# Performance work log

Hardware: AMD Instinct MI355X
Metric: run time of the kernel (lower is better)

## Reference

```python
import jax, jax.numpy as jnp
import numpy as np

N = 10000
E = 160000
F_IN = 64
HID = 128
HEADS = 8
NC = 3
NEG_SLOPE = 0.2
EPS = 1e-16


def setup_inputs() -> dict:
    key = jax.random.key(0)
    ks = jax.random.split(key, 12)
    p = lambda k, shape: jax.random.normal(k, shape, jnp.float32) * 0.1
    return {
        "x": jax.random.normal(ks[0], (N, F_IN), jnp.float32),
        "edge_index": jax.random.randint(ks[1], (2, E), 0, N),
        # conv1: F_IN -> 8 heads x 128, concat -> 1024
        "W1": p(ks[2], (F_IN, HEADS * HID)),
        "a_src1": p(ks[3], (HEADS, HID)),
        "a_dst1": p(ks[4], (HEADS, HID)),
        "b1": jnp.zeros((HEADS * HID,), jnp.float32),
        # conv2: 1024 -> 8 heads x 64, concat -> 512
        "W2": p(ks[5], (HEADS * HID, HEADS * (HID // 2))),
        "a_src2": p(ks[6], (HEADS, HID // 2)),
        "a_dst2": p(ks[7], (HEADS, HID // 2)),
        "b2": jnp.zeros((HEADS * (HID // 2),), jnp.float32),
        # conv3: 512 -> 1 head x 3, mean (concat=False)
        "W3": p(ks[8], (HEADS * (HID // 2), NC)),
        "a_src3": p(ks[9], (1, NC)),
        "a_dst3": p(ks[10], (1, NC)),
        "b3": jnp.zeros((NC,), jnp.float32),
    }


def gat_conv(x, src, dst, W, a_src, a_dst, b, concat):
    """PyG-style GATConv (eval mode, self-loops already in src/dst)."""
    n = x.shape[0]
    H, C = a_src.shape
    h = (x @ W).reshape(n, H, C)                      # [N, H, C]
    s_src = jnp.sum(h * a_src[None], axis=-1)         # [N, H]
    s_dst = jnp.sum(h * a_dst[None], axis=-1)         # [N, H]
    e = jax.nn.leaky_relu(s_src[src] + s_dst[dst], NEG_SLOPE)  # [E, H]
    # segment softmax over incoming edges per destination node
    m = jax.ops.segment_max(e, dst, num_segments=n)   # [N, H]
    ex = jnp.exp(e - m[dst])
    denom = jax.ops.segment_sum(ex, dst, num_segments=n)
    alpha = ex / (denom[dst] + EPS)                   # [E, H]
    msg = h[src] * alpha[:, :, None]                  # [E, H, C]
    out = jax.ops.segment_sum(msg, dst, num_segments=n)  # [N, H, C]
    out = out.reshape(n, H * C) if concat else out.mean(axis=1)
    return out + b


def reference(x, edge_index, W1, a_src1, a_dst1, b1, W2, a_src2, a_dst2, b2, W3, a_src3, a_dst3, b3):
    n = x.shape[0]
    loop = jnp.arange(n, dtype=edge_index.dtype)
    src = jnp.concatenate([edge_index[0], loop])
    dst = jnp.concatenate([edge_index[1], loop])
    h = gat_conv(x, src, dst, W1, a_src1, a_dst1, b1, True)
    h = jax.nn.elu(h)
    h = gat_conv(h, src, dst, W2, a_src2, a_dst2, b2, True)
    h = jax.nn.elu(h)
    h = gat_conv(h, src, dst, W3, a_src3, a_dst3, b3, False)
    return jax.nn.log_softmax(h, axis=1)
```

## Files before the change

kernel.cpp:

```cpp
#include <hip/hip_runtime.h>
#include <math.h>

#define NEG_SLOPE 0.2f
#define EPS_DEN 1e-16f

typedef __attribute__((ext_vector_type(8))) short bf16x8;
typedef __attribute__((ext_vector_type(4))) float f32x4;

__device__ inline unsigned short f2bf(float f) {
    unsigned u = __float_as_uint(f);
    return (unsigned short)((u + 0x7FFFu + ((u >> 16) & 1u)) >> 16);
}
__device__ inline float bflo(unsigned u) { return __uint_as_float(u << 16); }
__device__ inline float bfhi(unsigned u) { return __uint_as_float(u & 0xFFFF0000u); }

__global__ __launch_bounds__(256) void k_pre(const int* __restrict__ ei, int E, int Nn,
                                             int* __restrict__ counts,
                                             const float* __restrict__ x, short* __restrict__ A1, int Mp,
                                             const float* __restrict__ W1, short* __restrict__ B1t,
                                             const float* __restrict__ W2, short* __restrict__ B2t) {
    __shared__ float s[32][33];
    int t = threadIdx.x;
    int b = blockIdx.x;
    int ET = E + Nn;
    int etb = (ET + 255) / 256;
    int xb = (Mp * 64 + 255) / 256;
    if (b < etb) {
        int e = b * 256 + t;
        if (e < ET) {
            int d = (e < E) ? ei[E + e] : (e - E);
            atomicAdd(&counts[d], 1);
        }
        return;
    }
    b -= etb;
    if (b < xb) {
        int i = b * 256 + t;
        if (i < Mp * 64) {
            int row = i >> 6, c = i & 63;
            float v = (row < Nn) ? x[(size_t)row * 64 + c] : 0.f;
            A1[(size_t)row * 64 + c] = (short)f2bf(v);
        }
        return;
    }
    b -= xb;
    const float* W; short* Bt; int K, N, kb, nb;
    if (b < 64) {
        W = W1; Bt = B1t; K = 64; N = 1024;
        kb = b & 1; nb = b >> 1;
    } else {
        b -= 64;
        W = W2; Bt = B2t; K = 1024; N = 512;
        kb = b & 31; nb = b >> 5;
    }
    int k0 = kb * 32, n0 = nb * 32;
    int tx = t & 31, ty = t >> 5;
    for (int r = ty; r < 32; r += 8) s[r][tx] = W[(size_t)(k0 + r) * N + n0 + tx];
    __syncthreads();
    for (int r = ty; r < 32; r += 8) {
        float v = s[tx][r];
        Bt[(size_t)(n0 + r) * K + k0 + tx] = (short)f2bf(v);
    }
}

__global__ void k_scan(const int* __restrict__ counts, int Nn, int ET, int* __restrict__ row_off) {
    __shared__ int lds[256];
    int t = threadIdx.x;
    int chunk = (Nn + 255) / 256;
    int b0 = t * chunk, b1 = min(Nn, b0 + chunk);
    int s = 0;
    for (int i = b0; i < b1; i++) s += counts[i];
    lds[t] = s;
    __syncthreads();
    #pragma unroll
    for (int d = 1; d < 256; d <<= 1) {
        int v = (t >= d) ? lds[t - d] : 0;
        __syncthreads();
        lds[t] += v;
        __syncthreads();
    }
    int run = (t == 0) ? 0 : lds[t - 1];
    for (int i = b0; i < b1; i++) { row_off[i] = run; run += counts[i]; }
    if (t == 0) row_off[Nn] = ET;
}

__global__ void k_scatter(const int* __restrict__ ei, int E, int Nn,
                          const int* __restrict__ row_off, int* cursor, int* __restrict__ col) {
    int e = blockIdx.x * blockDim.x + threadIdx.x;
    int ET = E + Nn;
    if (e >= ET) return;
    int d = (e < E) ? ei[E + e] : (e - E);
    int s = (e < E) ? ei[e] : (e - E);
    int pos = atomicAdd(&cursor[d], 1);
    col[row_off[d] + pos] = s;
}

template<int HEADC>
__global__ __launch_bounds__(256) void k_mfma_w(const short* __restrict__ A,
                                                const short* __restrict__ B,
                                                unsigned short* __restrict__ C,
                                                const float* __restrict__ a_src,
                                                const float* __restrict__ a_dst,
                                                float* __restrict__ ssrc,
                                                float* __restrict__ sdst,
                                                int M, int N, int Ktot,
                                                int lda, int ldb) {
    __shared__ short As[64 * 32];
    __shared__ short Bs[128 * 32];
    __shared__ float sred[4][64][2];
    int t = threadIdx.x;
    int lane = t & 63;
    int wid = t >> 6;

    int nbx = N >> 7;
    int nb = gridDim.x;
    int q = nb >> 3, r = nb & 7;
    int xcd = blockIdx.x & 7, pos = blockIdx.x >> 3;
    int L = (xcd < r ? xcd * (q + 1) : r * (q + 1) + (xcd - r) * q) + pos;
    int bn = (L % nbx) * 128;
    int bm = (L / nbx) * 64;

    int wm = (wid & 1) * 32, wn = (wid >> 1) * 64;
    int fr = lane & 15, kq = lane >> 4;

    int srow = t >> 2, sslot = t & 3;
    int sko = ((sslot ^ ((srow >> 1) & 3)) << 3);

    f32x4 acc[2][4] = {};

    for (int k0 = 0; k0 < Ktot; k0 += 32) {
        {
            const short* sa = A + (size_t)(bm + srow) * lda + k0 + sko;
            short* da = As + (size_t)(wid << 6) * 8;
            __builtin_amdgcn_global_load_lds((const __attribute__((address_space(1))) void*)sa,
                                             (__attribute__((address_space(3))) void*)da, 16, 0, 0);
            #pragma unroll
            for (int qq = 0; qq < 2; qq++) {
                int v = qq * 256 + t;
                int rowb = v >> 2, slotb = v & 3;
                int skob = ((slotb ^ ((rowb >> 1) & 3)) << 3);
                const short* sb = B + (size_t)(bn + rowb) * ldb + k0 + skob;
                short* db = Bs + (size_t)(qq * 256 + (wid << 6)) * 8;
                __builtin_amdgcn_global_load_lds((const __attribute__((address_space(1))) void*)sb,
                                                 (__attribute__((address_space(3))) void*)db, 16, 0, 0);
            }
        }
        __syncthreads();
        bf16x8 af[2], bfv[4];
        #pragma unroll
        for (int i = 0; i < 2; i++) {
            int rowa = wm + i * 16 + fr;
            af[i] = *(const bf16x8*)(As + rowa * 32 + ((kq ^ ((rowa >> 1) & 3)) << 3));
        }
        #pragma unroll
        for (int j = 0; j < 4; j++) {
            int rowb = wn + j * 16 + fr;
            bfv[j] = *(const bf16x8*)(Bs + rowb * 32 + ((kq ^ ((rowb >> 1) & 3)) << 3));
        }
        #pragma unroll
        for (int i = 0; i < 2; i++)
            #pragma unroll
            for (int j = 0; j < 4; j++)
                acc[i][j] = __builtin_amdgcn_mfma_f32_16x16x32_bf16(af[i], bfv[j], acc[i][j], 0, 0, 0);
        __syncthreads();
    }
    #pragma unroll
    for (int i = 0; i < 2; i++) {
        int rbase = bm + wm + i * 16 + kq * 4;
        #pragma unroll
        for (int j = 0; j < 4; j++) {
            int colc = bn + wn + j * 16 + fr;
            #pragma unroll
            for (int rg = 0; rg < 4; rg++) {
                int rr = rbase + rg;
                if (rr < M) C[(size_t)rr * N + colc] = f2bf(acc[i][j][rg]);
            }
        }
    }
    float asv[4], adv[4];
    #pragma unroll
    for (int j = 0; j < 4; j++) {
        int colc = bn + wn + j * 16 + fr;
        asv[j] = a_src[colc];
        adv[j] = a_dst[colc];
    }
    float ps[8], pd[8];
    #pragma unroll
    for (int i = 0; i < 2; i++)
        #pragma unroll
        for (int rg = 0; rg < 4; rg++) {
            int k8 = i * 4 + rg;
            ps[k8] = acc[i][0][rg] * asv[0] + acc[i][1][rg] * asv[1]
                   + acc[i][2][rg] * asv[2] + acc[i][3][rg] * asv[3];
            pd[k8] = acc[i][0][rg] * adv[0] + acc[i][1][rg] * adv[1]
                   + acc[i][2][rg] * adv[2] + acc[i][3][rg] * adv[3];
        }
    #pragma unroll
    for (int k8 = 0; k8 < 8; k8++) {
        #pragma unroll
        for (int off = 1; off < 16; off <<= 1) {
            ps[k8] += __shfl_xor(ps[k8], off);
            pd[k8] += __shfl_xor(pd[k8], off);
        }
    }
    if (HEADC == 128) {
        if (fr == 0) {
            #pragma unroll
            for (int i = 0; i < 2; i++)
                #pragma unroll
                for (int rg = 0; rg < 4; rg++) {
                    int rl = wm + i * 16 + kq * 4 + rg;
                    sred[wid][rl][0] = ps[i * 4 + rg];
                    sred[wid][rl][1] = pd[i * 4 + rg];
                }
        }
        __syncthreads();
        if (wid < 2 && fr == 0) {
            int hh = bn >> 7;
            #pragma unroll
            for (int i = 0; i < 2; i++)
                #pragma unroll
                for (int rg = 0; rg < 4; rg++) {
                    int rl = wm + i * 16 + kq * 4 + rg;
                    int rr = bm + rl;
                    if (rr < M) {
                        ssrc[rr * 8 + hh] = sred[wid][rl][0] + sred[wid + 2][rl][0];
                        sdst[rr * 8 + hh] = sred[wid][rl][1] + sred[wid + 2][rl][1];
                    }
                }
        }
    } else {
        int hh = (bn + wn) >> 6;
        if (fr == 0) {
            #pragma unroll
            for (int i = 0; i < 2; i++)
                #pragma unroll
                for (int rg = 0; rg < 4; rg++) {
                    int rr = bm + wm + i * 16 + kq * 4 + rg;
                    if (rr < M) {
                        ssrc[rr * 8 + hh] = ps[i * 4 + rg];
                        sdst[rr * 8 + hh] = pd[i * 4 + rg];
                    }
                }
        }
    }
}

__global__ __launch_bounds__(256) void k_agg1_x(const unsigned short* __restrict__ hsrc,
                                                const float* __restrict__ ssrc,
                                                const float* __restrict__ sdst,
                                                const int* __restrict__ col,
                                                const int* __restrict__ row_off,
                                                const float* __restrict__ bias,
                                                unsigned short* __restrict__ osp,
                                                int Nn) {
    constexpr int D = 1024;
    int lane = threadIdx.x & 63;
    int wid = threadIdx.x >> 6;
    int xcd = blockIdx.x & 7, pos = blockIdx.x >> 3;
    int slice = xcd & 3;
    int n = pos * 8 + ((xcd >> 2) << 2) + wid;
    if (n >= Nn) return;
    int col0 = slice * 256 + lane * 4;
    int myhead = col0 >> 7;
    float sd = sdst[n * 8 + myhead];
    int beg = row_off[n], end = row_off[n + 1];
    const unsigned short* hbase = hsrc + col0;

    float acc[4] = {0.f, 0.f, 0.f, 0.f};
    float den = 0.f;
    #pragma unroll 4
    for (int j = beg; j < end; j++) {
        int cj = col[j];
        float s = ssrc[cj * 8 + myhead] + sd;
        s = (s >= 0.f) ? s : NEG_SLOPE * s;
        float ex = __expf(s);
        den += ex;
        uint2 u = *(const uint2*)(hbase + (size_t)cj * D);
        acc[0] += ex * bflo(u.x); acc[1] += ex * bfhi(u.x);
        acc[2] += ex * bflo(u.y); acc[3] += ex * bfhi(u.y);
    }
    float iv = 1.f / (den + EPS_DEN);
    float vals[4];
    #pragma unroll
    for (int v = 0; v < 4; v++) {
        float val = acc[v] * iv + bias[col0 + v];
        vals[v] = (val > 0.f) ? val : (__expf(val) - 1.f);
    }
    uint2 o;
    o.x = (unsigned)f2bf(vals[0]) | ((unsigned)f2bf(vals[1]) << 16);
    o.y = (unsigned)f2bf(vals[2]) | ((unsigned)f2bf(vals[3]) << 16);
    *(uint2*)(osp + (size_t)n * D + col0) = o;
}

__global__ __launch_bounds__(256) void k_agg2_l3(const unsigned short* __restrict__ hsrc,
                                                 const float* __restrict__ ssrc,
                                                 const float* __restrict__ sdst,
                                                 const int* __restrict__ col,
                                                 const int* __restrict__ row_off,
                                                 const float* __restrict__ bias,
                                                 const float* __restrict__ W3,
                                                 const float* __restrict__ as3,
                                                 const float* __restrict__ ad3,
                                                 float4* __restrict__ h3s,
                                                 float* __restrict__ sdst3,
                                                 int Nn) {
    constexpr int D = 512;
    __shared__ float cacc[2][64][9];
    int t = threadIdx.x;
    int lane = t & 63;
    int wid = t >> 6;
    int node_i = wid >> 1, half = wid & 1;
    int n = blockIdx.x * 2 + node_i;
    bool active = (n < Nn);
    int col0 = lane * 8;
    int myhead = lane >> 3;
    float acc[8] = {0.f, 0.f, 0.f, 0.f, 0.f, 0.f, 0.f, 0.f};
    float den = 0.f;
    if (active) {
        float sd = sdst[n * 8 + myhead];
        int beg = row_off[n], end = row_off[n + 1];
        const unsigned short* hbase = hsrc + col0;
        #pragma unroll 4
        for (int j = beg + half; j < end; j += 2) {
            int cj = col[j];
            float s = ssrc[cj * 8 + myhead] + sd;
            s = (s >= 0.f) ? s : NEG_SLOPE * s;
            float ex = __expf(s);
            den += ex;
            uint4 u = *(const uint4*)(hbase + (size_t)cj * D);
            acc[0] += ex * bflo(u.x); acc[1] += ex * bfhi(u.x);
            acc[2] += ex * bflo(u.y); acc[3] += ex * bfhi(u.y);
            acc[4] += ex * bflo(u.z); acc[5] += ex * bfhi(u.z);
            acc[6] += ex * bflo(u.w); acc[7] += ex * bfhi(u.w);
        }
    }
    if (half == 1) {
        #pragma unroll
        for (int v = 0; v < 8; v++) cacc[node_i][lane][v] = acc[v];
        cacc[node_i][lane][8] = den;
    }
    __syncthreads();
    if (half == 0 && active) {
        #pragma unroll
        for (int v = 0; v < 8; v++) acc[v] += cacc[node_i][lane][v];
        den += cacc[node_i][lane][8];
        float iv = 1.f / (den + EPS_DEN);
        float t0 = 0.f, t1 = 0.f, t2 = 0.f;
        #pragma unroll
        for (int v = 0; v < 8; v++) {
            float val = acc[v] * iv + bias[col0 + v];
            val = (val > 0.f) ? val : (__expf(val) - 1.f);
            const float* wp = W3 + (size_t)(col0 + v) * 3;
            t0 += val * wp[0];
            t1 += val * wp[1];
            t2 += val * wp[2];
        }
        #pragma unroll
        for (int off = 32; off >= 1; off >>= 1) {
            t0 += __shfl_xor(t0, off);
            t1 += __shfl_xor(t1, off);
            t2 += __shfl_xor(t2, off);
        }
        if (lane == 0) {
            float s3 = t0 * as3[0] + t1 * as3[1] + t2 * as3[2];
            h3s[n] = make_float4(t0, t1, t2, s3);
            sdst3[n] = t0 * ad3[0] + t1 * ad3[1] + t2 * ad3[2];
        }
    }
}

__global__ __launch_bounds__(256) void k_l3_fused(const float4* __restrict__ h3s,
                                                  const float* __restrict__ sdst, const int* __restrict__ col,
                                                  const int* __restrict__ row_off, const float* __restrict__ b3,
                                                  float* __restrict__ out, int Nn) {
    int n = blockIdx.x * 64 + (threadIdx.x >> 2);
    int l4 = threadIdx.x & 3;
    if (n >= Nn) return;
    int beg = row_off[n], end = row_off[n + 1];
    float sd = sdst[n];
    float den = 0.f, a0 = 0.f, a1 = 0.f, a2 = 0.f;
    for (int j = beg + l4; j < end; j += 4) {
        int sI = col[j];
        float4 v = h3s[sI];
        float s = v.w + sd;
        s = (s >= 0.f) ? s : NEG_SLOPE * s;
        float ex = __expf(s);
        den += ex;
        a0 += ex * v.x;
        a1 += ex * v.y;
        a2 += ex * v.z;
    }
    #pragma unroll
    for (int off = 1; off <= 2; off <<= 1) {
        den += __shfl_xor(den, off);
        a0 += __shfl_xor(a0, off);
        a1 += __shfl_xor(a1, off);
        a2 += __shfl_xor(a2, off);
    }
    if (l4 == 0) {
        float iv = 1.f / (den + EPS_DEN);
        float v0 = a0 * iv + b3[0], v1 = a1 * iv + b3[1], v2 = a2 * iv + b3[2];
        float m = fmaxf(v0, fmaxf(v1, v2));
        float l = logf(__expf(v0 - m) + __expf(v1 - m) + __expf(v2 - m));
        out[n * 3 + 0] = v0 - m - l;
        out[n * 3 + 1] = v1 - m - l;
        out[n * 3 + 2] = v2 - m - l;
    }
}

extern "C" void kernel_launch(void* const* d_in, const int* in_sizes, int n_in,
                              void* d_out, int out_size, void* d_ws, size_t ws_size,
                              hipStream_t stream) {
    (void)n_in; (void)out_size; (void)ws_size;
    const float* x   = (const float*)d_in[0];
    const int*   ei  = (const int*)d_in[1];
    const float* W1  = (const float*)d_in[2];
    const float* as1 = (const float*)d_in[3];
    const float* ad1 = (const float*)d_in[4];
    const float* b1  = (const float*)d_in[5];
    const float* W2  = (const float*)d_in[6];
    const float* as2 = (const float*)d_in[7];
    const float* ad2 = (const float*)d_in[8];
    const float* b2  = (const float*)d_in[9];
    const float* W3  = (const float*)d_in[10];
    const float* as3 = (const float*)d_in[11];
    const float* ad3 = (const float*)d_in[12];
    const float* b3  = (const float*)d_in[13];
    float* out = (float*)d_out;

    const int Nn = in_sizes[0] / 64;
    const int E  = in_sizes[1] / 2;
    const int ET = E + Nn;
    const int Mp = ((Nn + 127) / 128) * 128;

    char* ws = (char*)d_ws;
    size_t off = 0;
    auto alloc = [&](size_t bytes) -> void* {
        void* p = ws + off;
        off = (off + bytes + 255) & ~(size_t)255;
        return p;
    };
    unsigned short* hbuf = (unsigned short*)alloc((size_t)Mp * 1024 * 2);
    unsigned short* A2   = (unsigned short*)alloc((size_t)Mp * 1024 * 2);
    float4* h3s = (float4*)alloc((size_t)Nn * 16);
    short* A1   = (short*)alloc((size_t)Mp * 64 * 2);
    short* B1t  = (short*)alloc((size_t)1024 * 64 * 2);
    short* B2t  = (short*)alloc((size_t)512 * 1024 * 2);
    float* ssrc = (float*)alloc((size_t)Nn * 8 * 4);
    float* sdst = (float*)alloc((size_t)Nn * 8 * 4);
    float* ssrcB= (float*)alloc((size_t)Nn * 8 * 4);
    float* sdstB= (float*)alloc((size_t)Nn * 8 * 4);
    float* sdst3= (float*)alloc((size_t)Nn * 4);
    int* counts = (int*)alloc((size_t)Nn * 2 * 4);
    int* cursor = counts + Nn;
    int* row_off= (int*)alloc((size_t)(Nn + 1) * 4);
    int* colb   = (int*)alloc((size_t)ET * 4);

    hipMemsetAsync(counts, 0, (size_t)Nn * 2 * 4, stream);

    int etb = (ET + 255) / 256;
    int xb = (Mp * 64 + 255) / 256;
    int preb = etb + xb + 64 + 512;
    k_pre<<<preb, 256, 0, stream>>>(ei, E, Nn, counts, x, A1, Mp, W1, B1t, W2, B2t);
    k_scan<<<1, 256, 0, stream>>>(counts, Nn, ET, row_off);
    k_scatter<<<etb, 256, 0, stream>>>(ei, E, Nn, row_off, cursor, colb);

    {
        int nb = (1024 / 128) * (Mp / 64);
        k_mfma_w<128><<<nb, 256, 0, stream>>>(A1, B1t, hbuf, as1, ad1, ssrc, sdst,
                                              Nn, 1024, 64, 64, 64);
        int nblk = (Nn + 7) / 8 * 8;
        k_agg1_x<<<nblk, 256, 0, stream>>>(hbuf, ssrc, sdst, colb, row_off, b1, A2, Nn);
    }
    {
        int nb = (512 / 128) * (Mp / 64);
        k_mfma_w<64><<<nb, 256, 0, stream>>>((const short*)A2, B2t, hbuf, as2, ad2, ssrcB, sdstB,
                                             Nn, 512, 1024, 1024, 1024);
        k_agg2_l3<<<(Nn + 1) / 2, 256, 0, stream>>>(hbuf, ssrcB, sdstB, colb, row_off, b2,
                                                    W3, as3, ad3, h3s, sdst3, Nn);
    }
    k_l3_fused<<<(Nn + 63) / 64, 256, 0, stream>>>(h3s, sdst3, colb, row_off, b3, out, Nn);
}
```

Measured before the change: 162.9 us.

## Precompute per-edge attention exponentials and inverse denominators in a separate pass

```diff
diff --git a/kernel.cpp b/kernel.cpp
--- a/kernel.cpp
+++ b/kernel.cpp
@@ -246,9 +246,31 @@
     }
 }
 
+__global__ __launch_bounds__(256) void k_edge_ex(const float* __restrict__ ssrc,
+                                                 const float* __restrict__ sdst,
+                                                 const int* __restrict__ col,
+                                                 const int* __restrict__ row_off,
+                                                 float* __restrict__ exb,
+                                                 float* __restrict__ inv, int Nn) {
+    int p = blockIdx.x * blockDim.x + threadIdx.x;
+    if (p >= Nn * 8) return;
+    int n = p >> 3, h = p & 7;
+    int beg = row_off[n], end = row_off[n + 1];
+    float sd = sdst[p];
+    float den = 0.f;
+    for (int j = beg; j < end; j++) {
+        float s = ssrc[col[j] * 8 + h] + sd;
+        s = fmaxf(s, NEG_SLOPE * s);
+        float ex = __expf(s);
+        exb[(size_t)j * 8 + h] = ex;
+        den += ex;
+    }
+    inv[p] = 1.f / (den + EPS_DEN);
+}
+
 __global__ __launch_bounds__(256) void k_agg1_x(const unsigned short* __restrict__ hsrc,
-                                                const float* __restrict__ ssrc,
-                                                const float* __restrict__ sdst,
+                                                const float* __restrict__ exb,
+                                                const float* __restrict__ inv,
                                                 const int* __restrict__ col,
                                                 const int* __restrict__ row_off,
                                                 const float* __restrict__ bias,
@@ -263,24 +285,19 @@
     if (n >= Nn) return;
     int col0 = slice * 256 + lane * 4;
     int myhead = col0 >> 7;
-    float sd = sdst[n * 8 + myhead];
     int beg = row_off[n], end = row_off[n + 1];
     const unsigned short* hbase = hsrc + col0;
 
     float acc[4] = {0.f, 0.f, 0.f, 0.f};
-    float den = 0.f;
     #pragma unroll 4
     for (int j = beg; j < end; j++) {
         int cj = col[j];
-        float s = ssrc[cj * 8 + myhead] + sd;
-        s = (s >= 0.f) ? s : NEG_SLOPE * s;
-        float ex = __expf(s);
-        den += ex;
+        float ex = exb[(size_t)j * 8 + myhead];
         uint2 u = *(const uint2*)(hbase + (size_t)cj * D);
         acc[0] += ex * bflo(u.x); acc[1] += ex * bfhi(u.x);
         acc[2] += ex * bflo(u.y); acc[3] += ex * bfhi(u.y);
     }
-    float iv = 1.f / (den + EPS_DEN);
+    float iv = inv[n * 8 + myhead];
     float vals[4];
     #pragma unroll
     for (int v = 0; v < 4; v++) {
@@ -294,8 +311,8 @@
 }
 
 __global__ __launch_bounds__(256) void k_agg2_l3(const unsigned short* __restrict__ hsrc,
-                                                 const float* __restrict__ ssrc,
-                                                 const float* __restrict__ sdst,
+                                                 const float* __restrict__ exb,
+                                                 const float* __restrict__ inv,
                                                  const int* __restrict__ col,
                                                  const int* __restrict__ row_off,
                                                  const float* __restrict__ bias,
@@ -306,7 +323,7 @@
                                                  float* __restrict__ sdst3,
                                                  int Nn) {
     constexpr int D = 512;
-    __shared__ float cacc[2][64][9];
+    __shared__ float cacc[2][64][8];
     int t = threadIdx.x;
     int lane = t & 63;
     int wid = t >> 6;
@@ -316,18 +333,13 @@
     int col0 = lane * 8;
     int myhead = lane >> 3;
     float acc[8] = {0.f, 0.f, 0.f, 0.f, 0.f, 0.f, 0.f, 0.f};
-    float den = 0.f;
     if (active) {
-        float sd = sdst[n * 8 + myhead];
         int beg = row_off[n], end = row_off[n + 1];
         const unsigned short* hbase = hsrc + col0;
         #pragma unroll 4
         for (int j = beg + half; j < end; j += 2) {
             int cj = col[j];
-            float s = ssrc[cj * 8 + myhead] + sd;
-            s = (s >= 0.f) ? s : NEG_SLOPE * s;
-            float ex = __expf(s);
-            den += ex;
+            float ex = exb[(size_t)j * 8 + myhead];
             uint4 u = *(const uint4*)(hbase + (size_t)cj * D);
             acc[0] += ex * bflo(u.x); acc[1] += ex * bfhi(u.x);
             acc[2] += ex * bflo(u.y); acc[3] += ex * bfhi(u.y);
@@ -338,14 +350,12 @@
     if (half == 1) {
         #pragma unroll
         for (int v = 0; v < 8; v++) cacc[node_i][lane][v] = acc[v];
-        cacc[node_i][lane][8] = den;
     }
     __syncthreads();
     if (half == 0 && active) {
         #pragma unroll
         for (int v = 0; v < 8; v++) acc[v] += cacc[node_i][lane][v];
-        den += cacc[node_i][lane][8];
-        float iv = 1.f / (den + EPS_DEN);
+        float iv = inv[n * 8 + myhead];
         float t0 = 0.f, t1 = 0.f, t2 = 0.f;
         #pragma unroll
         for (int v = 0; v < 8; v++) {
@@ -384,7 +394,7 @@
         int sI = col[j];
         float4 v = h3s[sI];
         float s = v.w + sd;
-        s = (s >= 0.f) ? s : NEG_SLOPE * s;
+        s = fmaxf(s, NEG_SLOPE * s);
         float ex = __expf(s);
         den += ex;
         a0 += ex * v.x;
@@ -443,14 +453,14 @@
     };
     unsigned short* hbuf = (unsigned short*)alloc((size_t)Mp * 1024 * 2);
     unsigned short* A2   = (unsigned short*)alloc((size_t)Mp * 1024 * 2);
+    float* exb  = (float*)alloc((size_t)ET * 8 * 4);
     float4* h3s = (float4*)alloc((size_t)Nn * 16);
     short* A1   = (short*)alloc((size_t)Mp * 64 * 2);
     short* B1t  = (short*)alloc((size_t)1024 * 64 * 2);
     short* B2t  = (short*)alloc((size_t)512 * 1024 * 2);
     float* ssrc = (float*)alloc((size_t)Nn * 8 * 4);
     float* sdst = (float*)alloc((size_t)Nn * 8 * 4);
-    float* ssrcB= (float*)alloc((size_t)Nn * 8 * 4);
-    float* sdstB= (float*)alloc((size_t)Nn * 8 * 4);
+    float* inv  = (float*)alloc((size_t)Nn * 8 * 4);
     float* sdst3= (float*)alloc((size_t)Nn * 4);
     int* counts = (int*)alloc((size_t)Nn * 2 * 4);
     int* cursor = counts + Nn;
@@ -466,18 +476,22 @@
     k_scan<<<1, 256, 0, stream>>>(counts, Nn, ET, row_off);
     k_scatter<<<etb, 256, 0, stream>>>(ei, E, Nn, row_off, cursor, colb);
 
+    int nwh = (Nn * 8 + 255) / 256;
+
     {
         int nb = (1024 / 128) * (Mp / 64);
         k_mfma_w<128><<<nb, 256, 0, stream>>>(A1, B1t, hbuf, as1, ad1, ssrc, sdst,
                                               Nn, 1024, 64, 64, 64);
+        k_edge_ex<<<nwh, 256, 0, stream>>>(ssrc, sdst, colb, row_off, exb, inv, Nn);
         int nblk = (Nn + 7) / 8 * 8;
-        k_agg1_x<<<nblk, 256, 0, stream>>>(hbuf, ssrc, sdst, colb, row_off, b1, A2, Nn);
+        k_agg1_x<<<nblk, 256, 0, stream>>>(hbuf, exb, inv, colb, row_off, b1, A2, Nn);
     }
     {
         int nb = (512 / 128) * (Mp / 64);
-        k_mfma_w<64><<<nb, 256, 0, stream>>>((const short*)A2, B2t, hbuf, as2, ad2, ssrcB, sdstB,
+        k_mfma_w<64><<<nb, 256, 0, stream>>>((const short*)A2, B2t, hbuf, as2, ad2, ssrc, sdst,
                                              Nn, 512, 1024, 1024, 1024);
-        k_agg2_l3<<<(Nn + 1) / 2, 256, 0, stream>>>(hbuf, ssrcB, sdstB, colb, row_off, b2,
+        k_edge_ex<<<nwh, 256, 0, stream>>>(ssrc, sdst, colb, row_off, exb, inv, Nn);
+        k_agg2_l3<<<(Nn + 1) / 2, 256, 0, stream>>>(hbuf, exb, inv, colb, row_off, b2,
                                                     W3, as3, ad3, h3s, sdst3, Nn);
     }
     k_l3_fused<<<(Nn + 63) / 64, 256, 0, stream>>>(h3s, sdst3, colb, row_off, b3, out, Nn);
```

After: 184.8 us. 13.4% more time.

## Batch edge score computation across lanes and broadcast via shuffles in aggregation kernels

Applied to the files above, without the earlier changes.

```diff
diff --git a/kernel.cpp b/kernel.cpp
--- a/kernel.cpp
+++ b/kernel.cpp
@@ -262,25 +262,36 @@
     int n = pos * 8 + ((xcd >> 2) << 2) + wid;
     if (n >= Nn) return;
     int col0 = slice * 256 + lane * 4;
-    int myhead = col0 >> 7;
+    int myhead = (slice << 1) | (lane >> 5);
+    int l32 = lane & 31;
     float sd = sdst[n * 8 + myhead];
     int beg = row_off[n], end = row_off[n + 1];
     const unsigned short* hbase = hsrc + col0;
 
     float acc[4] = {0.f, 0.f, 0.f, 0.f};
-    float den = 0.f;
-    #pragma unroll 4
-    for (int j = beg; j < end; j++) {
-        int cj = col[j];
-        float s = ssrc[cj * 8 + myhead] + sd;
-        s = (s >= 0.f) ? s : NEG_SLOPE * s;
-        float ex = __expf(s);
-        den += ex;
-        uint2 u = *(const uint2*)(hbase + (size_t)cj * D);
-        acc[0] += ex * bflo(u.x); acc[1] += ex * bfhi(u.x);
-        acc[2] += ex * bflo(u.y); acc[3] += ex * bfhi(u.y);
-    }
-    float iv = 1.f / (den + EPS_DEN);
+    float denp = 0.f;
+    for (int j0 = beg; j0 < end; j0 += 32) {
+        int nb2 = min(32, end - j0);
+        float exm = 0.f; int cjm = 0;
+        if (l32 < nb2) {
+            cjm = col[j0 + l32];
+            float s = ssrc[cjm * 8 + myhead] + sd;
+            s = fmaxf(s, NEG_SLOPE * s);
+            exm = __expf(s);
+        }
+        denp += exm;
+        #pragma unroll 4
+        for (int i = 0; i < nb2; i++) {
+            float ex = __shfl(exm, i, 32);
+            int cj = __shfl(cjm, i, 32);
+            uint2 u = *(const uint2*)(hbase + (size_t)cj * D);
+            acc[0] += ex * bflo(u.x); acc[1] += ex * bfhi(u.x);
+            acc[2] += ex * bflo(u.y); acc[3] += ex * bfhi(u.y);
+        }
+    }
+    #pragma unroll
+    for (int off = 16; off >= 1; off >>= 1) denp += __shfl_xor(denp, off, 32);
+    float iv = 1.f / (denp + EPS_DEN);
     float vals[4];
     #pragma unroll
     for (int v = 0; v < 4; v++) {
@@ -306,28 +317,32 @@
                                                  float* __restrict__ sdst3,
                                                  int Nn) {
     constexpr int D = 512;
-    __shared__ float cacc[2][64][9];
-    int t = threadIdx.x;
-    int lane = t & 63;
-    int wid = t >> 6;
-    int node_i = wid >> 1, half = wid & 1;
-    int n = blockIdx.x * 2 + node_i;
-    bool active = (n < Nn);
+    int lane = threadIdx.x & 63;
+    int n = blockIdx.x * 4 + (threadIdx.x >> 6);
+    if (n >= Nn) return;
     int col0 = lane * 8;
     int myhead = lane >> 3;
+    int l8 = lane & 7;
+    float sd = sdst[n * 8 + myhead];
+    int beg = row_off[n], end = row_off[n + 1];
+    const unsigned short* hbase = hsrc + col0;
+
     float acc[8] = {0.f, 0.f, 0.f, 0.f, 0.f, 0.f, 0.f, 0.f};
-    float den = 0.f;
-    if (active) {
-        float sd = sdst[n * 8 + myhead];
-        int beg = row_off[n], end = row_off[n + 1];
-        const unsigned short* hbase = hsrc + col0;
+    float denp = 0.f;
+    for (int j0 = beg; j0 < end; j0 += 8) {
+        int nb2 = min(8, end - j0);
+        float exm = 0.f; int cjm = 0;
+        if (l8 < nb2) {
+            cjm = col[j0 + l8];
+            float s = ssrc[cjm * 8 + myhead] + sd;
+            s = fmaxf(s, NEG_SLOPE * s);
+            exm = __expf(s);
+        }
+        denp += exm;
         #pragma unroll 4
-        for (int j = beg + half; j < end; j += 2) {
-            int cj = col[j];
-            float s = ssrc[cj * 8 + myhead] + sd;
-            s = (s >= 0.f) ? s : NEG_SLOPE * s;
-            float ex = __expf(s);
-            den += ex;
+        for (int i = 0; i < nb2; i++) {
+            float ex = __shfl(exm, i, 8);
+            int cj = __shfl(cjm, i, 8);
             uint4 u = *(const uint4*)(hbase + (size_t)cj * D);
             acc[0] += ex * bflo(u.x); acc[1] += ex * bfhi(u.x);
             acc[2] += ex * bflo(u.y); acc[3] += ex * bfhi(u.y);
@@ -335,38 +350,29 @@
             acc[6] += ex * bflo(u.w); acc[7] += ex * bfhi(u.w);
         }
     }
-    if (half == 1) {
-        #pragma unroll
-        for (int v = 0; v < 8; v++) cacc[node_i][lane][v] = acc[v];
-        cacc[node_i][lane][8] = den;
-    }
-    __syncthreads();
-    if (half == 0 && active) {
-        #pragma unroll
-        for (int v = 0; v < 8; v++) acc[v] += cacc[node_i][lane][v];
-        den += cacc[node_i][lane][8];
-        float iv = 1.f / (den + EPS_DEN);
-        float t0 = 0.f, t1 = 0.f, t2 = 0.f;
-        #pragma unroll
-        for (int v = 0; v < 8; v++) {
-            float val = acc[v] * iv + bias[col0 + v];
-            val = (val > 0.f) ? val : (__expf(val) - 1.f);
-            const float* wp = W3 + (size_t)(col0 + v) * 3;
-            t0 += val * wp[0];
-            t1 += val * wp[1];
-            t2 += val * wp[2];
-        }
-        #pragma unroll
-        for (int off = 32; off >= 1; off >>= 1) {
-            t0 += __shfl_xor(t0, off);
-            t1 += __shfl_xor(t1, off);
-            t2 += __shfl_xor(t2, off);
-        }
-        if (lane == 0) {
-            float s3 = t0 * as3[0] + t1 * as3[1] + t2 * as3[2];
-            h3s[n] = make_float4(t0, t1, t2, s3);
-            sdst3[n] = t0 * ad3[0] + t1 * ad3[1] + t2 * ad3[2];
-        }
+    #pragma unroll
+    for (int off = 4; off >= 1; off >>= 1) denp += __shfl_xor(denp, off, 8);
+    float iv = 1.f / (denp + EPS_DEN);
+    float t0 = 0.f, t1 = 0.f, t2 = 0.f;
+    #pragma unroll
+    for (int v = 0; v < 8; v++) {
+        float val = acc[v] * iv + bias[col0 + v];
+        val = (val > 0.f) ? val : (__expf(val) - 1.f);
+        const float* wp = W3 + (size_t)(col0 + v) * 3;
+        t0 += val * wp[0];
+        t1 += val * wp[1];
+        t2 += val * wp[2];
+    }
+    #pragma unroll
+    for (int off = 32; off >= 1; off >>= 1) {
+        t0 += __shfl_xor(t0, off);
+        t1 += __shfl_xor(t1, off);
+        t2 += __shfl_xor(t2, off);
+    }
+    if (lane == 0) {
+        float s3 = t0 * as3[0] + t1 * as3[1] + t2 * as3[2];
+        h3s[n] = make_float4(t0, t1, t2, s3);
+        sdst3[n] = t0 * ad3[0] + t1 * ad3[1] + t2 * ad3[2];
     }
 }
 
@@ -384,7 +390,7 @@
         int sI = col[j];
         float4 v = h3s[sI];
         float s = v.w + sd;
-        s = (s >= 0.f) ? s : NEG_SLOPE * s;
+        s = fmaxf(s, NEG_SLOPE * s);
         float ex = __expf(s);
         den += ex;
         a0 += ex * v.x;
@@ -477,7 +483,7 @@
         int nb = (512 / 128) * (Mp / 64);
         k_mfma_w<64><<<nb, 256, 0, stream>>>((const short*)A2, B2t, hbuf, as2, ad2, ssrcB, sdstB,
                                              Nn, 512, 1024, 1024, 1024);
-        k_agg2_l3<<<(Nn + 1) / 2, 256, 0, stream>>>(hbuf, ssrcB, sdstB, colb, row_off, b2,
+        k_agg2_l3<<<(Nn + 3) / 4, 256, 0, stream>>>(hbuf, ssrcB, sdstB, colb, row_off, b2,
                                                     W3, as3, ad3, h3s, sdst3, Nn);
     }
     k_l3_fused<<<(Nn + 63) / 64, 256, 0, stream>>>(h3s, sdst3, colb, row_off, b3, out, Nn);
```

Result: slower. 176.6 us (+8.4%).
